# Kernel optimization log

Hardware: AMD Instinct MI355X
Metric: run time of the kernel (lower is better)

The kernel has to match this reference:

```python
import jax, jax.numpy as jnp
import numpy as np

DIM = 1024
HEADS = 8
NUM_KEYS = 256
TOPK = 32
D_HEAD = DIM // HEADS
BATCH = 2
SEQ = 2048


def setup_inputs() -> dict:
    key = jax.random.key(0)
    ks = jax.random.split(key, 5)
    x = jax.random.normal(ks[0], (BATCH, SEQ, DIM), jnp.float32)
    # nn.Linear(dim, 2*dim, bias=False): weight (2*dim, dim)
    Wq = jax.random.normal(ks[1], (2 * DIM, DIM), jnp.float32) * (DIM ** -0.5)
    # nn.Parameter(torch.randn(heads, num_keys, 2, d_head))
    keys = jax.random.normal(ks[2], (HEADS, NUM_KEYS, 2, D_HEAD), jnp.float32)
    # nn.Parameter(torch.randn(heads, num_keys**2, d_head))
    values = jax.random.normal(ks[3], (HEADS, NUM_KEYS ** 2, D_HEAD), jnp.float32)
    # nn.Linear(dim, dim): weight (dim, dim), bias (dim,)
    Wo = jax.random.normal(ks[4], (DIM, DIM), jnp.float32) * (DIM ** -0.5)
    bo = jnp.zeros((DIM,), jnp.float32)
    return {"x": x, "Wq": Wq, "keys": keys, "values": values, "Wo": Wo, "bo": bo}


def reference(x, Wq, keys, values, Wo, bo):
    b, t, e = x.shape
    h, dh, k, nk = HEADS, D_HEAD, TOPK, NUM_KEYS
    # to_queries + chunk(2, dim=-1) + stack -> (2, b, t, h, d_head)
    q = x @ Wq.T                                    # (b, t, 2*dim)
    q = q.reshape(b, t, 2, e).transpose(2, 0, 1, 3)  # (2, b, t, dim), matches chunk+stack
    q = q.reshape(2, b, t, h, dh)
    # dual sub-key scores: (b, h, t, 2, num_keys)
    dots = jnp.einsum('pbthd,hnpd->bhtpn', q, keys)
    # top-k over num_keys per sub-key
    scores, indices = jax.lax.top_k(dots, k)         # (b, h, t, 2, k)
    # faithful to source: chunk(2, dim=2) splits the TIME axis
    th = t // 2
    s0, s1 = scores[:, :, :th], scores[:, :, th:]
    i0, i1 = indices[:, :, :th], indices[:, :, th:]
    # Cartesian combination: (b, h, t//2, 2, k, k) -> (b, h, t, k*k)
    all_scores = (s0[..., :, None] + s1[..., None, :]).reshape(b, h, t, k * k)
    all_indices = (i0[..., :, None] * nk + i1[..., None, :]).reshape(b, h, t, k * k)
    # final top-k over the k^2 candidates
    final_scores, final_idx = jax.lax.top_k(all_scores, k)   # (b, h, t, k)
    value_indices = jnp.take_along_axis(all_indices, final_idx, axis=-1)  # (b, h, t, k)
    attn = jax.nn.softmax(final_scores, axis=-1)
    # gather values per head: values (h, nk^2, dh), idx (b, h, t, k) -> (b, h, t, k, dh)
    sel = jax.vmap(lambda v, idx: v[idx], in_axes=(0, 1), out_axes=1)(values, value_indices)
    out = jnp.einsum('bhtk,bhtkd->bhtd', attn, sel)  # weighted sum over top-k
    out = out.transpose(0, 2, 1, 3).reshape(b, t, e)
    return out @ Wo.T + bo
```

## Files before the change

### kernel.cpp

```cpp
#include <hip/hip_runtime.h>

typedef unsigned int u32;
typedef unsigned long long u64;
typedef _Float16 f16;
typedef __attribute__((ext_vector_type(4))) _Float16 f16x4;
typedef __attribute__((ext_vector_type(8))) _Float16 f16x8;
typedef __attribute__((ext_vector_type(4))) float f32x4;
typedef const __attribute__((address_space(1))) void* gp_t;
typedef __attribute__((address_space(3))) void* lp_t;

#define TSEQ 2048

__device__ __forceinline__ u32 f2sort(float f) {
  u32 u = __float_as_uint(f);
  return u ^ ((u32)((int)u >> 31) | 0x80000000u);
}
__device__ __forceinline__ float sort2f(u32 u) {
  u ^= (u & 0x80000000u) ? 0x80000000u : 0xFFFFFFFFu;
  return __uint_as_float(u);
}

__device__ __forceinline__ void glds16(const f16* g, f16* l) {
  __builtin_amdgcn_global_load_lds((gp_t)g, (lp_t)l, 16, 0, 0);
}

__device__ __forceinline__ u32 dppmax16(u32 v) {
  u32 t;
  t = (u32)__builtin_amdgcn_update_dpp(0, (int)v, 0x111, 0xF, 0xF, true);
  v = v > t ? v : t;
  t = (u32)__builtin_amdgcn_update_dpp(0, (int)v, 0x112, 0xF, 0xF, true);
  v = v > t ? v : t;
  t = (u32)__builtin_amdgcn_update_dpp(0, (int)v, 0x114, 0xF, 0xF, true);
  v = v > t ? v : t;
  t = (u32)__builtin_amdgcn_update_dpp(0, (int)v, 0x118, 0xF, 0xF, true);
  v = v > t ? v : t;
  return (u32)__builtin_amdgcn_ds_swizzle((int)v, 0x1F0);
}
__device__ __forceinline__ float dppsum16(float v) {
  float t;
  t = __int_as_float(
      __builtin_amdgcn_update_dpp(0, __float_as_int(v), 0x111, 0xF, 0xF, true));
  v += t;
  t = __int_as_float(
      __builtin_amdgcn_update_dpp(0, __float_as_int(v), 0x112, 0xF, 0xF, true));
  v += t;
  t = __int_as_float(
      __builtin_amdgcn_update_dpp(0, __float_as_int(v), 0x114, 0xF, 0xF, true));
  v += t;
  t = __int_as_float(
      __builtin_amdgcn_update_dpp(0, __float_as_int(v), 0x118, 0xF, 0xF, true));
  v += t;
  return __int_as_float(__builtin_amdgcn_ds_swizzle(__float_as_int(v), 0x1F0));
}

__global__ __launch_bounds__(256) void cvt_all(
    const float* __restrict__ x, const float* __restrict__ wq,
    const float* __restrict__ wo, const float* __restrict__ ky,
    const float* __restrict__ vl, f16* __restrict__ xd, f16* __restrict__ wqd,
    f16* __restrict__ wod, f16* __restrict__ kyd, f16* __restrict__ vld) {
  int g = blockIdx.x * 256 + threadIdx.x;
  const float* s;
  f16* d;
  int off;
  if (g >= 1966080)     { s = vl; d = vld; off = g - 1966080; }
  else if (g < 1048576) { s = x;  d = xd;  off = g; }
  else if (g < 1572864) { s = wq; d = wqd; off = g - 1048576; }
  else if (g < 1835008) { s = wo; d = wod; off = g - 1572864; }
  else                  { s = ky; d = kyd; off = g - 1835008; }
  float4 v = ((const float4*)s)[off];
  f16x4 o;
  o[0] = (f16)v.x; o[1] = (f16)v.y; o[2] = (f16)v.z; o[3] = (f16)v.w;
  ((f16x4*)d)[off] = o;
}

__global__ __launch_bounds__(256) void gemm_f16(
    const f16* __restrict__ A, int lda, const f16* __restrict__ B, int ldb,
    const float* __restrict__ bias, void* __restrict__ Cv, int ldc, int K,
    int c_f16) {
  __shared__ f16 As[128 * 32];
  __shared__ f16 Bs[128 * 32];
  const int tid = threadIdx.x;
  const int lane = tid & 63, wave = tid >> 6;
  const int m0 = blockIdx.y << 7, n0 = blockIdx.x << 7;
  const int c0 = wave * 128 + lane, c1 = c0 + 64;
  const int r0 = c0 >> 2, s0 = c0 & 3;
  const int r1 = c1 >> 2, s1 = c1 & 3;
  const f16* Ab = A + (size_t)m0 * lda;
  const f16* Bb = B + (size_t)n0 * ldb;
  const int fm = lane & 15, fq = lane >> 4, fk = fq << 3;
  const int wm = (wave >> 1) << 6, wn = (wave & 1) << 6;
  f32x4 acc[4][4] = {};
  for (int k0 = 0; k0 < K; k0 += 32) {
    __syncthreads();
    glds16(Ab + (size_t)r0 * lda + k0 + s0 * 8, As + (size_t)c0 * 8 - lane * 8);
    glds16(Ab + (size_t)r1 * lda + k0 + s1 * 8, As + (size_t)c1 * 8 - lane * 8);
    glds16(Bb + (size_t)r0 * ldb + k0 + s0 * 8, Bs + (size_t)c0 * 8 - lane * 8);
    glds16(Bb + (size_t)r1 * ldb + k0 + s1 * 8, Bs + (size_t)c1 * 8 - lane * 8);
    __syncthreads();
    f16x8 af[4], bf[4];
#pragma unroll
    for (int mi = 0; mi < 4; mi++)
      af[mi] = *(const f16x8*)&As[(wm + mi * 16 + fm) * 32 + fk];
#pragma unroll
    for (int nj = 0; nj < 4; nj++)
      bf[nj] = *(const f16x8*)&Bs[(wn + nj * 16 + fm) * 32 + fk];
#pragma unroll
    for (int mi = 0; mi < 4; mi++)
#pragma unroll
      for (int nj = 0; nj < 4; nj++)
        acc[mi][nj] = __builtin_amdgcn_mfma_f32_16x16x32_f16(
            af[mi], bf[nj], acc[mi][nj], 0, 0, 0);
  }
  if (c_f16) {
    f16* C = (f16*)Cv;
#pragma unroll
    for (int mi = 0; mi < 4; mi++)
#pragma unroll
      for (int r = 0; r < 4; r++) {
        int row = m0 + wm + mi * 16 + fq * 4 + r;
        f16* cp = C + (size_t)row * ldc + n0 + wn + fm;
#pragma unroll
        for (int nj = 0; nj < 4; nj++) cp[nj * 16] = (f16)acc[mi][nj][r];
      }
  } else {
    float* C = (float*)Cv;
    float bb[4];
#pragma unroll
    for (int nj = 0; nj < 4; nj++)
      bb[nj] = bias ? bias[n0 + wn + nj * 16 + fm] : 0.f;
#pragma unroll
    for (int mi = 0; mi < 4; mi++)
#pragma unroll
      for (int r = 0; r < 4; r++) {
        int row = m0 + wm + mi * 16 + fq * 4 + r;
        float* cp = C + (size_t)row * ldc + n0 + wn + fm;
#pragma unroll
        for (int nj = 0; nj < 4; nj++) cp[nj * 16] = acc[mi][nj][r] + bb[nj];
      }
  }
}

__global__ __launch_bounds__(256) void dots_topk1(
    const f16* __restrict__ Q,
    const f16* __restrict__ keysf,
    float* __restrict__ s1s, int* __restrict__ s1i) {
  __shared__ f16 As[64 * 32];
  __shared__ f16 Bs[256 * 32];
  const int tid = threadIdx.x;
  const int lane = tid & 63, wave = tid >> 6;
  const int z = blockIdx.x;
  const int h = z >> 1, p = z & 1;
  const int m0 = blockIdx.y << 6;
  const f16* Aq = Q + (size_t)m0 * 2048 + p * 1024 + h * 128;
  const f16* Bk = keysf + ((size_t)h * 512 + p) * 128;
  const int cA = wave * 64 + lane;
  const int rA = cA >> 2, sA = cA & 3;
  const int fm = lane & 15, fq = lane >> 4, fk = fq << 3;
  f32x4 acc[16] = {};
  for (int k0 = 0; k0 < 128; k0 += 32) {
    __syncthreads();
    glds16(Aq + (size_t)rA * 2048 + k0 + sA * 8, As + (size_t)cA * 8 - lane * 8);
#pragma unroll
    for (int c = 0; c < 4; c++) {
      int cB = (wave * 4 + c) * 64 + lane;
      int rB = cB >> 2, sB = cB & 3;
      glds16(Bk + (size_t)rB * 256 + k0 + sB * 8,
             Bs + (size_t)cB * 8 - lane * 8);
    }
    __syncthreads();
    f16x8 af = *(const f16x8*)&As[(wave * 16 + fm) * 32 + fk];
#pragma unroll
    for (int j = 0; j < 16; j++) {
      f16x8 bf = *(const f16x8*)&Bs[(j * 16 + fm) * 32 + fk];
      acc[j] = __builtin_amdgcn_mfma_f32_16x16x32_f16(af, bf, acc[j], 0, 0, 0);
    }
  }
  for (int r = 0; r < 4; r++) {
    u32 key[16];
#pragma unroll
    for (int j = 0; j < 16; j++)
      key[j] = (f2sort(acc[j][r]) & ~0xFFu) | (u32)((j << 4) | fm);
    u32 g0 = 0, g1 = 0;
    for (int it = 0; it < 32; it++) {
      u32 lm = key[0];
#pragma unroll
      for (int j = 1; j < 16; j++) lm = key[j] > lm ? key[j] : lm;
      u32 gm = dppmax16(lm);
#pragma unroll
      for (int j = 0; j < 16; j++) key[j] = (key[j] == gm) ? 0u : key[j];
      bool sel = (fm == (it & 15));
      if (it < 16) g0 = sel ? gm : g0;
      else         g1 = sel ? gm : g1;
    }
    int m = m0 + wave * 16 + (fq << 2) + r;
    int b = m >> 11, t = m & 2047;
    size_t orow = ((((size_t)(b * 8 + h)) * TSEQ + t) * 2 + p) * 32;
    s1s[orow + fm] = sort2f(g0 & ~0xFFu);
    s1s[orow + fm + 16] = sort2f(g1 & ~0xFFu);
    s1i[orow + fm] = (int)(g0 & 0xFFu);
    s1i[orow + fm + 16] = (int)(g1 & 0xFFu);
  }
}

__global__ __launch_bounds__(256) void topk2_gather(
    const float* __restrict__ s1s, const int* __restrict__ s1i,
    const f16* __restrict__ valf, f16* __restrict__ headout) {
  __shared__ unsigned short cand[128];
  __shared__ float s0sh[16][32];
  __shared__ float s1sh[16][32];
  __shared__ int i0sh[16][32];
  __shared__ int i1sh[16][32];
  __shared__ int vtab[16][32];
  __shared__ float wtab[16][32];
  const int tid = threadIdx.x;
  if (tid < 128) {
    int c = tid;
    unsigned short enc = 0xFFFF;
    if (c < 119) {
      int rem = c, i = 0;
      for (i = 0; i < 32; i++) {
        int cnt = 32 / (i + 1);
        if (rem < cnt) break;
        rem -= cnt;
      }
      enc = (unsigned short)((i << 5) | rem);
    }
    cand[tid] = enc;
  }
  const int rloc = tid >> 4;
  const int l = tid & 15;
  const int row = blockIdx.x * 16 + rloc;
  const int b = row >> 14;
  const int h = (row >> 11) & 7;
  const int t = row & 2047;
  const int tt = t >> 1, p = t & 1;
  size_t rbase = (size_t)(b * 8 + h) * TSEQ;
  size_t base0 = ((rbase + tt) * 2 + p) * 32;
  size_t base1 = ((rbase + tt + 1024) * 2 + p) * 32;
  s0sh[rloc][l] = s1s[base0 + l];
  s0sh[rloc][l + 16] = s1s[base0 + l + 16];
  s1sh[rloc][l] = s1s[base1 + l];
  s1sh[rloc][l + 16] = s1s[base1 + l + 16];
  i0sh[rloc][l] = s1i[base0 + l];
  i0sh[rloc][l + 16] = s1i[base0 + l + 16];
  i1sh[rloc][l] = s1i[base1 + l];
  i1sh[rloc][l + 16] = s1i[base1 + l + 16];
  __syncthreads();
  u32 key[8];
#pragma unroll
  for (int s = 0; s < 8; s++) {
    int c = l + 16 * s;
    unsigned short e = cand[c];
    u32 kk = 0u;
    if (e != 0xFFFF) {
      float v = s0sh[rloc][e >> 5] + s1sh[rloc][e & 31];
      kk = (f2sort(v) & ~0xFFu) | (u32)c;
    }
    key[s] = kk;
  }
  u32 g0 = 0, g1 = 0;
  for (int it = 0; it < 32; it++) {
    u32 lm = key[0];
#pragma unroll
    for (int s = 1; s < 8; s++) lm = key[s] > lm ? key[s] : lm;
    u32 gm = dppmax16(lm);
#pragma unroll
    for (int s = 0; s < 8; s++) key[s] = (key[s] == gm) ? 0u : key[s];
    bool sel = (l == (it & 15));
    if (it < 16) g0 = sel ? gm : g0;
    else         g1 = sel ? gm : g1;
  }
  float sc0 = sort2f(g0 & ~0xFFu);
  float sc1 = sort2f(g1 & ~0xFFu);
  unsigned short e0c = cand[g0 & 0xFFu];
  unsigned short e1c = cand[g1 & 0xFFu];
  int vidx0 = i0sh[rloc][e0c >> 5] * 256 + i1sh[rloc][e0c & 31];
  int vidx1 = i0sh[rloc][e1c >> 5] * 256 + i1sh[rloc][e1c & 31];
  float mx = __int_as_float(
      __builtin_amdgcn_ds_swizzle(__float_as_int(sc0), 0x010));
  float e0 = __expf(sc0 - mx);
  float e1 = __expf(sc1 - mx);
  float inv = 1.0f / dppsum16(e0 + e1);
  vtab[rloc][l] = vidx0;
  vtab[rloc][l + 16] = vidx1;
  wtab[rloc][l] = e0 * inv;
  wtab[rloc][l + 16] = e1 * inv;
  const f16* vb = valf + (((size_t)h) << 16) * 128 + l * 8;
  float accf[8] = {};
#pragma unroll 8
  for (int k = 0; k < 32; k++) {
    int vi = vtab[rloc][k];
    float wk = wtab[rloc][k];
    f16x8 vv = *(const f16x8*)(vb + (size_t)vi * 128);
#pragma unroll
    for (int j = 0; j < 8; j++) accf[j] += wk * (float)vv[j];
  }
  f16x8 o;
#pragma unroll
  for (int j = 0; j < 8; j++) o[j] = (f16)accf[j];
  f16* op = headout + (size_t)(b * TSEQ + t) * 1024 + h * 128 + l * 8;
  *(f16x8*)op = o;
}

extern "C" void kernel_launch(void* const* d_in, const int* in_sizes, int n_in,
                              void* d_out, int out_size, void* d_ws,
                              size_t ws_size, hipStream_t stream) {
  const float* x    = (const float*)d_in[0];
  const float* Wq   = (const float*)d_in[1];
  const float* keys = (const float*)d_in[2];
  const float* vals = (const float*)d_in[3];
  const float* Wo   = (const float*)d_in[4];
  const float* bo   = (const float*)d_in[5];
  float* out = (float*)d_out;
  char* ws = (char*)d_ws;
  f16*   xf   = (f16*)(ws);
  f16*   wqf  = (f16*)(ws + (size_t)(8u << 20));
  f16*   wof  = (f16*)(ws + (size_t)(12u << 20));
  f16*   kyf  = (f16*)(ws + (size_t)(14u << 20));
  f16*   Qf   = (f16*)(ws + (size_t)(16u << 20));
  float* s1s  = (float*)(ws + (size_t)(32u << 20));
  int*   s1i  = (int*)(ws + (size_t)(40u << 20));
  f16*   hof  = (f16*)(ws + (size_t)(48u << 20));
  f16*   valf = (f16*)(ws + (size_t)(64u << 20));

  cvt_all<<<dim3(73216), 256, 0, stream>>>(x, Wq, Wo, keys, vals, xf, wqf, wof,
                                           kyf, valf);
  gemm_f16<<<dim3(16, 32), 256, 0, stream>>>(xf, 1024, wqf, 1024, nullptr, Qf,
                                             2048, 1024, 1);
  dots_topk1<<<dim3(16, 64), 256, 0, stream>>>(Qf, kyf, s1s, s1i);
  topk2_gather<<<dim3(32768 / 16), 256, 0, stream>>>(s1s, s1i, valf, hof);
  gemm_f16<<<dim3(8, 32), 256, 0, stream>>>(hof, 1024, wof, 1024, bo, out,
                                            1024, 1024, 0);
}
```

Measured before the change: 567.3 us.

## Gather fp32 values directly instead of converting the value table each call

The per-call fp16 conversion of the large values table is removed: the conversion kernel now handles only x, Wq, Wo and the keys, and the gather kernel reads fp32 values directly with two float4 loads per row. This avoids streaming the whole value table through a read-and-write pass when only a sparse subset of rows is ever touched. The cost is twice the bytes per gathered row. The DPP reductions switch to row-rotate patterns so every lane ends with the result without a swizzle broadcast, and the per-lane max scans become balanced trees to shorten dependency chains.

```diff
diff --git a/kernel.cpp b/kernel.cpp
--- a/kernel.cpp
+++ b/kernel.cpp
@@ -24,46 +24,47 @@
   __builtin_amdgcn_global_load_lds((gp_t)g, (lp_t)l, 16, 0, 0);
 }
 
+__device__ __forceinline__ u32 umax2(u32 a, u32 b) { return a > b ? a : b; }
+
 __device__ __forceinline__ u32 dppmax16(u32 v) {
   u32 t;
-  t = (u32)__builtin_amdgcn_update_dpp(0, (int)v, 0x111, 0xF, 0xF, true);
+  t = (u32)__builtin_amdgcn_update_dpp(0, (int)v, 0x128, 0xF, 0xF, true);
   v = v > t ? v : t;
-  t = (u32)__builtin_amdgcn_update_dpp(0, (int)v, 0x112, 0xF, 0xF, true);
+  t = (u32)__builtin_amdgcn_update_dpp(0, (int)v, 0x124, 0xF, 0xF, true);
   v = v > t ? v : t;
-  t = (u32)__builtin_amdgcn_update_dpp(0, (int)v, 0x114, 0xF, 0xF, true);
+  t = (u32)__builtin_amdgcn_update_dpp(0, (int)v, 0x122, 0xF, 0xF, true);
   v = v > t ? v : t;
-  t = (u32)__builtin_amdgcn_update_dpp(0, (int)v, 0x118, 0xF, 0xF, true);
+  t = (u32)__builtin_amdgcn_update_dpp(0, (int)v, 0x121, 0xF, 0xF, true);
   v = v > t ? v : t;
-  return (u32)__builtin_amdgcn_ds_swizzle((int)v, 0x1F0);
+  return v;
 }
 __device__ __forceinline__ float dppsum16(float v) {
   float t;
   t = __int_as_float(
-      __builtin_amdgcn_update_dpp(0, __float_as_int(v), 0x111, 0xF, 0xF, true));
+      __builtin_amdgcn_update_dpp(0, __float_as_int(v), 0x128, 0xF, 0xF, true));
   v += t;
   t = __int_as_float(
-      __builtin_amdgcn_update_dpp(0, __float_as_int(v), 0x112, 0xF, 0xF, true));
+      __builtin_amdgcn_update_dpp(0, __float_as_int(v), 0x124, 0xF, 0xF, true));
   v += t;
   t = __int_as_float(
-      __builtin_amdgcn_update_dpp(0, __float_as_int(v), 0x114, 0xF, 0xF, true));
+      __builtin_amdgcn_update_dpp(0, __float_as_int(v), 0x122, 0xF, 0xF, true));
   v += t;
   t = __int_as_float(
-      __builtin_amdgcn_update_dpp(0, __float_as_int(v), 0x118, 0xF, 0xF, true));
+      __builtin_amdgcn_update_dpp(0, __float_as_int(v), 0x121, 0xF, 0xF, true));
   v += t;
-  return __int_as_float(__builtin_amdgcn_ds_swizzle(__float_as_int(v), 0x1F0));
+  return v;
 }
 
 __global__ __launch_bounds__(256) void cvt_all(
     const float* __restrict__ x, const float* __restrict__ wq,
     const float* __restrict__ wo, const float* __restrict__ ky,
-    const float* __restrict__ vl, f16* __restrict__ xd, f16* __restrict__ wqd,
-    f16* __restrict__ wod, f16* __restrict__ kyd, f16* __restrict__ vld) {
+    f16* __restrict__ xd, f16* __restrict__ wqd, f16* __restrict__ wod,
+    f16* __restrict__ kyd) {
   int g = blockIdx.x * 256 + threadIdx.x;
   const float* s;
   f16* d;
   int off;
-  if (g >= 1966080)     { s = vl; d = vld; off = g - 1966080; }
-  else if (g < 1048576) { s = x;  d = xd;  off = g; }
+  if (g < 1048576)      { s = x;  d = xd;  off = g; }
   else if (g < 1572864) { s = wq; d = wqd; off = g - 1048576; }
   else if (g < 1835008) { s = wo; d = wod; off = g - 1572864; }
   else                  { s = ky; d = kyd; off = g - 1835008; }
@@ -182,9 +183,13 @@
       key[j] = (f2sort(acc[j][r]) & ~0xFFu) | (u32)((j << 4) | fm);
     u32 g0 = 0, g1 = 0;
     for (int it = 0; it < 32; it++) {
-      u32 lm = key[0];
-#pragma unroll
-      for (int j = 1; j < 16; j++) lm = key[j] > lm ? key[j] : lm;
+      u32 t0 = umax2(key[0], key[1]), t1 = umax2(key[2], key[3]);
+      u32 t2 = umax2(key[4], key[5]), t3 = umax2(key[6], key[7]);
+      u32 t4 = umax2(key[8], key[9]), t5 = umax2(key[10], key[11]);
+      u32 t6 = umax2(key[12], key[13]), t7 = umax2(key[14], key[15]);
+      t0 = umax2(t0, t1); t2 = umax2(t2, t3);
+      t4 = umax2(t4, t5); t6 = umax2(t6, t7);
+      u32 lm = umax2(umax2(t0, t2), umax2(t4, t6));
       u32 gm = dppmax16(lm);
 #pragma unroll
       for (int j = 0; j < 16; j++) key[j] = (key[j] == gm) ? 0u : key[j];
@@ -204,7 +209,7 @@
 
 __global__ __launch_bounds__(256) void topk2_gather(
     const float* __restrict__ s1s, const int* __restrict__ s1i,
-    const f16* __restrict__ valf, f16* __restrict__ headout) {
+    const float* __restrict__ valf, f16* __restrict__ headout) {
   __shared__ unsigned short cand[128];
   __shared__ float s0sh[16][32];
   __shared__ float s1sh[16][32];
@@ -260,9 +265,9 @@
   }
   u32 g0 = 0, g1 = 0;
   for (int it = 0; it < 32; it++) {
-    u32 lm = key[0];
-#pragma unroll
-    for (int s = 1; s < 8; s++) lm = key[s] > lm ? key[s] : lm;
+    u32 t0 = umax2(key[0], key[1]), t1 = umax2(key[2], key[3]);
+    u32 t2 = umax2(key[4], key[5]), t3 = umax2(key[6], key[7]);
+    u32 lm = umax2(umax2(t0, t1), umax2(t2, t3));
     u32 gm = dppmax16(lm);
 #pragma unroll
     for (int s = 0; s < 8; s++) key[s] = (key[s] == gm) ? 0u : key[s];
@@ -285,15 +290,19 @@
   vtab[rloc][l + 16] = vidx1;
   wtab[rloc][l] = e0 * inv;
   wtab[rloc][l + 16] = e1 * inv;
-  const f16* vb = valf + (((size_t)h) << 16) * 128 + l * 8;
+  const float* vb = valf + (((size_t)h) << 23) + (size_t)l * 8;
   float accf[8] = {};
 #pragma unroll 8
   for (int k = 0; k < 32; k++) {
     int vi = vtab[rloc][k];
     float wk = wtab[rloc][k];
-    f16x8 vv = *(const f16x8*)(vb + (size_t)vi * 128);
-#pragma unroll
-    for (int j = 0; j < 8; j++) accf[j] += wk * (float)vv[j];
+    const float4* vp = (const float4*)(vb + (size_t)vi * 128);
+    float4 v0 = vp[0];
+    float4 v1 = vp[1];
+    accf[0] += wk * v0.x; accf[1] += wk * v0.y;
+    accf[2] += wk * v0.z; accf[3] += wk * v0.w;
+    accf[4] += wk * v1.x; accf[5] += wk * v1.y;
+    accf[6] += wk * v1.z; accf[7] += wk * v1.w;
   }
   f16x8 o;
 #pragma unroll
@@ -321,14 +330,12 @@
   float* s1s  = (float*)(ws + (size_t)(32u << 20));
   int*   s1i  = (int*)(ws + (size_t)(40u << 20));
   f16*   hof  = (f16*)(ws + (size_t)(48u << 20));
-  f16*   valf = (f16*)(ws + (size_t)(64u << 20));
-
-  cvt_all<<<dim3(73216), 256, 0, stream>>>(x, Wq, Wo, keys, vals, xf, wqf, wof,
-                                           kyf, valf);
+
+  cvt_all<<<dim3(7680), 256, 0, stream>>>(x, Wq, Wo, keys, xf, wqf, wof, kyf);
   gemm_f16<<<dim3(16, 32), 256, 0, stream>>>(xf, 1024, wqf, 1024, nullptr, Qf,
                                              2048, 1024, 1);
   dots_topk1<<<dim3(16, 64), 256, 0, stream>>>(Qf, kyf, s1s, s1i);
-  topk2_gather<<<dim3(32768 / 16), 256, 0, stream>>>(s1s, s1i, valf, hof);
+  topk2_gather<<<dim3(32768 / 16), 256, 0, stream>>>(s1s, s1i, vals, hof);
   gemm_f16<<<dim3(8, 32), 256, 0, stream>>>(hof, 1024, wof, 1024, bo, out,
                                             1024, 1024, 0);
 }
```

Result: faster. 530.8 us (-6.4%).
